# Kernel optimization log

Measured on AMD Instinct MI355X. Metric: run time of the kernel, lower is better.

Reference implementation:

```python
import jax, jax.numpy as jnp
import numpy as np

B, N, D, E, L = 4, 256, 128, 64, 3  # batch, nodes, node_dim, edge_dim, num_layers
LN_EPS = 1e-5


def setup_inputs() -> dict:
    key = jax.random.key(0)
    ks = jax.random.split(key, 12)

    def w(k, shape, fan_in):
        return jax.random.normal(k, shape, dtype=jnp.float32) / np.float32(np.sqrt(fan_in))

    return {
        "node_features": jax.random.normal(ks[0], (B, N, D), dtype=jnp.float32),
        "adjacency": jax.random.uniform(ks[1], (B, N, N), dtype=jnp.float32),
        # per-layer edge network: Linear(2D->E), ReLU, Linear(E->E)
        "ew1": w(ks[2], (L, 2 * D, E), 2 * D), "eb1": jnp.zeros((L, E), jnp.float32),
        "ew2": w(ks[3], (L, E, E), E),         "eb2": jnp.zeros((L, E), jnp.float32),
        # per-layer message network: Linear(D+E->2D), ReLU, Linear(2D->D)
        "mw1": w(ks[4], (L, D + E, 2 * D), D + E), "mb1": jnp.zeros((L, 2 * D), jnp.float32),
        "mw2": w(ks[5], (L, 2 * D, D), 2 * D),     "mb2": jnp.zeros((L, D), jnp.float32),
        # per-layer update network: Linear(2D->2D), ReLU, Linear(2D->D)
        "uw1": w(ks[6], (L, 2 * D, 2 * D), 2 * D), "ub1": jnp.zeros((L, 2 * D), jnp.float32),
        "uw2": w(ks[7], (L, 2 * D, D), 2 * D),     "ub2": jnp.zeros((L, D), jnp.float32),
        # per-layer LayerNorm
        "ln_g": jnp.ones((L, D), jnp.float32), "ln_b": jnp.zeros((L, D), jnp.float32),
    }


def _layernorm(x, g, b):
    mu = jnp.mean(x, axis=-1, keepdims=True)
    var = jnp.mean(jnp.square(x - mu), axis=-1, keepdims=True)
    return (x - mu) * jax.lax.rsqrt(var + LN_EPS) * g + b


def _forward(node_features, adjacency, ew1, eb1, ew2, eb2, mw1, mb1, mw2, mb2,
             uw1, ub1, uw2, ub2, ln_g, ln_b):
    x = node_features  # [B,N,D]
    for l in range(L):
        # Edge features: edge_input[b,i,j] = cat(x[b,i], x[b,j]); first Linear split to
        # avoid materializing [B,N,N,2D]: cat @ W == x_i @ W_top + x_j @ W_bot.
        w_top, w_bot = ew1[l][:D], ew1[l][D:]
        eh = jax.nn.relu(
            jnp.einsum('bid,de->bie', x, w_top)[:, :, None, :]
            + jnp.einsum('bjd,de->bje', x, w_bot)[:, None, :, :]
            + eb1[l]
        )  # [B,N,N,E]
        edge_feat = jnp.einsum('bije,ef->bijf', eh, ew2[l]) + eb2[l]  # [B,N,N,E]

        # GraphConvLayer: message_input[b,i,j] = cat(x[b,i], edge_feat[b,i,j])
        mw_top, mw_bot = mw1[l][:D], mw1[l][D:]
        mh = jax.nn.relu(
            jnp.einsum('bid,dh->bih', x, mw_top)[:, :, None, :]
            + jnp.einsum('bije,eh->bijh', edge_feat, mw_bot)
            + mb1[l]
        )  # [B,N,N,2D]
        message = jnp.einsum('bijh,hd->bijd', mh, mw2[l]) + mb2[l]  # [B,N,N,D]
        # adjacency-weighted sum over neighbors j (per-node torch loop, vectorized)
        messages = jnp.einsum('bij,bijd->bid', adjacency, message)  # [B,N,D]

        upd_in = jnp.concatenate([x, messages], axis=-1)  # [B,N,2D]
        uh = jax.nn.relu(jnp.einsum('bih,hk->bik', upd_in, uw1[l]) + ub1[l])
        x_new = jnp.einsum('bik,kd->bid', uh, uw2[l]) + ub2[l]  # [B,N,D]

        x = _layernorm(x + x_new, ln_g[l], ln_b[l])
    return x


def reference(node_features, adjacency, ew1, eb1, ew2, eb2, mw1, mb1, mw2, mb2,
              uw1, ub1, uw2, ub2, ln_g, ln_b):
    return _forward(node_features, adjacency, ew1, eb1, ew2, eb2, mw1, mb1, mw2,
                    mb2, uw1, ub1, uw2, ub2, ln_g, ln_b)
```

## Files before the change

kernel.cpp:

```cpp
#include <hip/hip_runtime.h>
#include <hip/hip_bf16.h>


constexpr int cB = 4, cN = 256, cD = 128, cE = 64, cL = 3, cH = 256;
constexpr int RT = 4;
#define LN_EPSF 1e-5f

typedef __attribute__((ext_vector_type(8))) short bf8;
typedef __attribute__((ext_vector_type(4))) float f4;

__device__ __forceinline__ ushort f2bf(float f) {
    uint u = __float_as_uint(f);
    u += 0x7FFFu + ((u >> 16) & 1u);
    return (ushort)(u >> 16);
}

__global__ __launch_bounds__(256) void kW(const float* __restrict__ ew2,
                                          const float* __restrict__ eb2,
                                          const float* __restrict__ mw1,
                                          ushort* __restrict__ W2f,
                                          float* __restrict__ BS2) {
    int bx = blockIdx.x, l = bx >> 3, f0 = (bx & 7) * 8;
    int h = threadIdx.x;
    const float* ew2l = ew2 + l * cE * cE;
    const float* eb2l = eb2 + l * cE;
    const float* mbot = mw1 + l * (cD + cE) * cH + cD * cH;
    float acc[8];
#pragma unroll
    for (int f = 0; f < 8; ++f) acc[f] = 0.f;
    float bacc = 0.f;
    for (int e = 0; e < cE; ++e) {
        float m = mbot[e * cH + h];
        if (f0 == 0) bacc += eb2l[e] * m;
#pragma unroll
        for (int f = 0; f < 8; ++f) acc[f] += ew2l[(f0 + f) * cE + e] * m;
    }
    ushort* W2fl = W2f + l * cE * cH;
    int ht = h >> 4, hc = h & 15;
#pragma unroll
    for (int f = 0; f < 8; ++f) {
        int ff = f0 + f;
        int kc = ff >> 5, lg = (ff >> 3) & 3, e = ff & 7;
        W2fl[((ht * 2 + kc) * 64 + lg * 16 + hc) * 8 + e] = f2bf(acc[f]);
    }
    if (f0 == 0) BS2[l * cH + h] = bacc;
}

__device__ __forceinline__ void proj_1024(const float (*xs)[cD],
                                          float (*ph4)[RT][cH],
                                          float (*pm8)[RT][cD],
                                          int r0, int t,
                                          const float* __restrict__ ew1,
                                          const float* __restrict__ eb1,
                                          const float* __restrict__ mw1,
                                          const float* __restrict__ mb1,
                                          const float* __restrict__ bs2,
                                          float* __restrict__ P1,
                                          float* __restrict__ P2,
                                          float* __restrict__ P3, int nl) {
    {
        int col = t & 255, kc = t >> 8;
        const float* mw1n = mw1 + nl * (cD + cE) * cH;
        float a[RT];
#pragma unroll
        for (int r = 0; r < RT; ++r) a[r] = 0.f;
        for (int k = kc * 32; k < kc * 32 + 32; ++k) {
            float w = mw1n[k * cH + col];
#pragma unroll
            for (int r = 0; r < RT; ++r) a[r] += xs[r][k] * w;
        }
#pragma unroll
        for (int r = 0; r < RT; ++r) ph4[kc][r][col] = a[r];
    }
    {
        int cc = t & 127, kc = t >> 7;
        int which = cc >> 6, e = cc & 63;
        const float* ew1n = ew1 + nl * 2 * cD * cE + which * cD * cE;
        float a[RT];
#pragma unroll
        for (int r = 0; r < RT; ++r) a[r] = 0.f;
        for (int k = kc * 16; k < kc * 16 + 16; ++k) {
            float w = ew1n[k * cE + e];
#pragma unroll
            for (int r = 0; r < RT; ++r) a[r] += xs[r][k] * w;
        }
#pragma unroll
        for (int r = 0; r < RT; ++r) pm8[kc][r][cc] = a[r];
    }
    __syncthreads();
    {
        int r = t >> 8, col = t & 255;
        float v = mb1[nl * cH + col] + bs2[nl * cH + col];
#pragma unroll
        for (int kc = 0; kc < 4; ++kc) v += ph4[kc][r][col];
        P3[(r0 + r) * cH + col] = v;
    }
    if (t < 512) {
        int r = t >> 7, cc = t & 127, which = cc >> 6, e = cc & 63;
        float v = which ? 0.f : eb1[nl * cE + e];
#pragma unroll
        for (int kc = 0; kc < 8; ++kc) v += pm8[kc][r][cc];
        (which ? P2 : P1)[(r0 + r) * cE + e] = v;
    }
}

__global__ __launch_bounds__(1024) void kP(const float* __restrict__ x,
                                           const float* __restrict__ ew1,
                                           const float* __restrict__ eb1,
                                           const float* __restrict__ mw1,
                                           const float* __restrict__ mb1,
                                           const float* __restrict__ bs2,
                                           float* __restrict__ P1,
                                           float* __restrict__ P2,
                                           float* __restrict__ P3) {
    __shared__ float xs[RT][cD];
    __shared__ float ph4[4][RT][cH];
    __shared__ float pm8[8][RT][cD];
    int r0 = blockIdx.x * RT, t = threadIdx.x;
    if (t < 512) {
        int r = t >> 7, d = t & 127;
        xs[r][d] = x[(r0 + r) * cD + d];
    }
    __syncthreads();
    proj_1024(xs, ph4, pm8, r0, t, ew1, eb1, mw1, mb1, bs2, P1, P2, P3, 0);
}

__global__ __launch_bounds__(256, 8) void kB(const float* __restrict__ P1,
                                             const float* __restrict__ P2,
                                             const float* __restrict__ P3,
                                             const float* __restrict__ adj,
                                             const ushort* __restrict__ W2f,
                                             float* __restrict__ Sp,
                                             float* __restrict__ AsumP, int l) {
    __shared__ float sP3[cH];
    __shared__ float sS[4][cH];
    __shared__ float sAs[4];
    int bx = blockIdx.x, bn = bx >> 1, half = bx & 1;
    int t = threadIdx.x, w = t >> 6, ln = t & 63, g = ln >> 4, c = ln & 15;
    int b = bn >> 8;
    int jw = half * 128 + w * 32;

    sP3[t] = P3[bn * cH + t];

    const float* adjr = adj + bn * cN + jw;
    float adjv[2][4];
    float asum = 0.f;
#pragma unroll
    for (int jt = 0; jt < 2; ++jt)
#pragma unroll
        for (int q = 0; q < 4; ++q) {
            float a = adjr[jt * 16 + g * 4 + q];
            adjv[jt][q] = a;
            asum += a;
        }
    asum += __shfl_xor(asum, 16);
    asum += __shfl_xor(asum, 32);

    const float* p1p = P1 + bn * cE;
    f4 p1lo[2], p1hi[2];
#pragma unroll
    for (int kc = 0; kc < 2; ++kc) {
        p1lo[kc] = *(const f4*)(p1p + kc * 32 + g * 8);
        p1hi[kc] = *(const f4*)(p1p + kc * 32 + g * 8 + 4);
    }

    bf8 af[2][2];
#pragma unroll
    for (int jt = 0; jt < 2; ++jt) {
        const float* p2r = P2 + (b * cN + jw + jt * 16 + c) * cE;
#pragma unroll
        for (int kc = 0; kc < 2; ++kc) {
            f4 v0 = *(const f4*)(p2r + kc * 32 + g * 8);
            f4 v1 = *(const f4*)(p2r + kc * 32 + g * 8 + 4);
            bf8 a;
#pragma unroll
            for (int e = 0; e < 4; ++e) {
                float x0 = v0[e] + p1lo[kc][e]; x0 = x0 > 0.f ? x0 : 0.f;
                float x1 = v1[e] + p1hi[kc][e]; x1 = x1 > 0.f ? x1 : 0.f;
                a[e]     = (short)f2bf(x0);
                a[e + 4] = (short)f2bf(x1);
            }
            af[jt][kc] = a;
        }
    }
    __syncthreads();

    const ushort* W2l = W2f + l * cE * cH;
    bf8 nb0 = *(const bf8*)(W2l + (0 * 64 + ln) * 8);
    bf8 nb1 = *(const bf8*)(W2l + (1 * 64 + ln) * 8);
    for (int ht = 0; ht < 16; ++ht) {
        bf8 b0 = nb0, b1 = nb1;
        if (ht < 15) {
            nb0 = *(const bf8*)(W2l + (((ht + 1) * 2 + 0) * 64 + ln) * 8);
            nb1 = *(const bf8*)(W2l + (((ht + 1) * 2 + 1) * 64 + ln) * 8);
        }
        float p3v = sP3[ht * 16 + c];
        float sp = 0.f;
#pragma unroll
        for (int jt = 0; jt < 2; ++jt) {
            f4 acc = {0.f, 0.f, 0.f, 0.f};
            acc = __builtin_amdgcn_mfma_f32_16x16x32_bf16(af[jt][0], b0, acc, 0, 0, 0);
            acc = __builtin_amdgcn_mfma_f32_16x16x32_bf16(af[jt][1], b1, acc, 0, 0, 0);
#pragma unroll
            for (int q = 0; q < 4; ++q) {
                float mh = p3v + acc[q];
                mh = mh > 0.f ? mh : 0.f;
                sp += adjv[jt][q] * mh;
            }
        }
        sp += __shfl_xor(sp, 16);
        sp += __shfl_xor(sp, 32);
        if (ln < 16) sS[w][ht * 16 + c] = sp;
    }
    if (ln == 0) sAs[w] = asum;
    __syncthreads();
    Sp[bx * cH + t] = sS[0][t] + sS[1][t] + sS[2][t] + sS[3][t];
    if (t == 0) AsumP[bx] = sAs[0] + sAs[1] + sAs[2] + sAs[3];
}

__global__ __launch_bounds__(1024) void kU(const float* __restrict__ x_in,
                                           float* __restrict__ x_out,
                                           const float* __restrict__ Sp,
                                           const float* __restrict__ AsumP,
                                           const float* __restrict__ mw2,
                                           const float* __restrict__ mb2,
                                           const float* __restrict__ uw1,
                                           const float* __restrict__ ub1,
                                           const float* __restrict__ uw2,
                                           const float* __restrict__ ub2,
                                           const float* __restrict__ lng,
                                           const float* __restrict__ lnb,
                                           float* __restrict__ out,
                                           const float* __restrict__ ew1,
                                           const float* __restrict__ eb1,
                                           const float* __restrict__ mw1,
                                           const float* __restrict__ mb1,
                                           const float* __restrict__ bs2,
                                           float* __restrict__ P1,
                                           float* __restrict__ P2,
                                           float* __restrict__ P3,
                                           int l, int last) {
    __shared__ float sS[RT][cH];
    __shared__ float uin[RT][cH];
    __shared__ float uh[RT][cH];
    __shared__ float ph4[4][RT][cH];
    __shared__ float pm8[8][RT][cD];
    __shared__ float yb[RT][cD];
    __shared__ float xs[RT][cD];
    __shared__ float atots[RT];
    __shared__ float rs1h[RT][2], rs2h[RT][2];
    int r0 = blockIdx.x * RT, t = threadIdx.x;

    {
        int r = t >> 8, k = t & 255;
        sS[r][k] = Sp[(2 * (r0 + r)) * cH + k] + Sp[(2 * (r0 + r) + 1) * cH + k];
    }
    if (t < RT) atots[t] = AsumP[2 * (r0 + t)] + AsumP[2 * (r0 + t) + 1];
    if (t < 512) {
        int r = t >> 7, d = t & 127;
        uin[r][d] = x_in[(r0 + r) * cD + d];
    }
    __syncthreads();

    {
        int c = t & 127, kc = t >> 7;
        const float* mw2l = mw2 + l * cH * cD;
        float a[RT];
#pragma unroll
        for (int r = 0; r < RT; ++r) a[r] = 0.f;
        for (int k = kc * 32; k < kc * 32 + 32; ++k) {
            float w = mw2l[k * cD + c];
#pragma unroll
            for (int r = 0; r < RT; ++r) a[r] += sS[r][k] * w;
        }
#pragma unroll
        for (int r = 0; r < RT; ++r) pm8[kc][r][c] = a[r];
    }
    __syncthreads();
    if (t < 512) {
        int r = t >> 7, c = t & 127;
        float m = atots[r] * mb2[l * cD + c];
#pragma unroll
        for (int kc = 0; kc < 8; ++kc) m += pm8[kc][r][c];
        uin[r][cD + c] = m;
    }
    __syncthreads();

    {
        int col = t & 255, kc = t >> 8;
        const float* uw1l = uw1 + l * cH * cH;
        float a[RT];
#pragma unroll
        for (int r = 0; r < RT; ++r) a[r] = 0.f;
        for (int k = kc * 64; k < kc * 64 + 64; ++k) {
            float w = uw1l[k * cH + col];
#pragma unroll
            for (int r = 0; r < RT; ++r) a[r] += uin[r][k] * w;
        }
#pragma unroll
        for (int r = 0; r < RT; ++r) ph4[kc][r][col] = a[r];
    }
    __syncthreads();
    {
        int r = t >> 8, col = t & 255;
        float v = ub1[l * cH + col];
#pragma unroll
        for (int kc = 0; kc < 4; ++kc) v += ph4[kc][r][col];
        uh[r][col] = v > 0.f ? v : 0.f;
    }
    __syncthreads();

    {
        int c = t & 127, kc = t >> 7;
        const float* uw2l = uw2 + l * cH * cD;
        float a[RT];
#pragma unroll
        for (int r = 0; r < RT; ++r) a[r] = 0.f;
        for (int k = kc * 32; k < kc * 32 + 32; ++k) {
            float w = uw2l[k * cD + c];
#pragma unroll
            for (int r = 0; r < RT; ++r) a[r] += uh[r][k] * w;
        }
#pragma unroll
        for (int r = 0; r < RT; ++r) pm8[kc][r][c] = a[r];
    }
    __syncthreads();
    if (t < 512) {
        int r = t >> 7, c = t & 127;
        float v = uin[r][c] + ub2[l * cD + c];
#pragma unroll
        for (int kc = 0; kc < 8; ++kc) v += pm8[kc][r][c];
        yb[r][c] = v;
    }
    __syncthreads();

    if (t < 512) {
        int r = t >> 7, q = t & 127;
        float y = yb[r][q];
        float s1 = y, s2 = y * y;
#pragma unroll
        for (int o = 1; o < 64; o <<= 1) { s1 += __shfl_xor(s1, o); s2 += __shfl_xor(s2, o); }
        if ((t & 63) == 0) { rs1h[r][q >> 6] = s1; rs2h[r][q >> 6] = s2; }
    }
    __syncthreads();
    if (t < 512) {
        int r = t >> 7, q = t & 127;
        float tot = rs1h[r][0] + rs1h[r][1];
        float tq  = rs2h[r][0] + rs2h[r][1];
        float mu  = tot * (1.f / cD);
        float var = tq * (1.f / cD) - mu * mu;
        float inv = rsqrtf(var + LN_EPSF);
        float res = (yb[r][q] - mu) * inv * lng[l * cD + q] + lnb[l * cD + q];
        x_out[(r0 + r) * cD + q] = res;
        xs[r][q] = res;
        if (last) out[(r0 + r) * cD + q] = res;
    }
    if (last) return;
    __syncthreads();

    proj_1024(xs, ph4, pm8, r0, t, ew1, eb1, mw1, mb1, bs2, P1, P2, P3, l + 1);
}

extern "C" void kernel_launch(void* const* d_in, const int* in_sizes, int n_in,
                              void* d_out, int out_size, void* d_ws, size_t ws_size,
                              hipStream_t stream) {
    (void)in_sizes; (void)n_in; (void)out_size; (void)ws_size;
    const float* nf  = (const float*)d_in[0];
    const float* adj = (const float*)d_in[1];
    const float* ew1 = (const float*)d_in[2];
    const float* eb1 = (const float*)d_in[3];
    const float* ew2 = (const float*)d_in[4];
    const float* eb2 = (const float*)d_in[5];
    const float* mw1 = (const float*)d_in[6];
    const float* mb1 = (const float*)d_in[7];
    const float* mw2 = (const float*)d_in[8];
    const float* mb2 = (const float*)d_in[9];
    const float* uw1 = (const float*)d_in[10];
    const float* ub1 = (const float*)d_in[11];
    const float* uw2 = (const float*)d_in[12];
    const float* ub2 = (const float*)d_in[13];
    const float* lng = (const float*)d_in[14];
    const float* lnb = (const float*)d_in[15];
    float* out = (float*)d_out;

    float* xbuf  = (float*)d_ws;
    float* P1    = xbuf + cB * cN * cD;
    float* P2    = P1   + cB * cN * cE;
    float* P3    = P2   + cB * cN * cE;
    float* Sp    = P3   + cB * cN * cH;
    float* AsumP = Sp   + 2 * cB * cN * cH;
    float* BS2   = AsumP + 2 * cB * cN;
    ushort* W2f  = (ushort*)(BS2 + cL * cH);

    kW<<<cL * 8, 256, 0, stream>>>(ew2, eb2, mw1, W2f, BS2);
    kP<<<cB * cN / RT, 1024, 0, stream>>>(nf, ew1, eb1, mw1, mb1, BS2, P1, P2, P3);
    for (int l = 0; l < cL; ++l) {
        kB<<<cB * cN * 2, 256, 0, stream>>>(P1, P2, P3, adj, W2f, Sp, AsumP, l);
        kU<<<cB * cN / RT, 1024, 0, stream>>>((l == 0) ? nf : xbuf, xbuf, Sp, AsumP,
                                              mw2, mb2, uw1, ub1, uw2, ub2, lng, lnb, out,
                                              ew1, eb1, mw1, mb1, BS2, P1, P2, P3,
                                              l, l == cL - 1);
    }
}
```

Before: 125.0 us.

## Split kB neighbor range into four blocks and defer cross-lane reductions

The edge/message kernel now launches four blocks per node instead of two, so each wave handles 16 neighbors (one MFMA tile) instead of 32. The bias is folded into the MFMA accumulator init, the 16 per-tile partial sums are kept in registers, and the shuffle reductions are batched after a fully unrolled loop. The update kernel sums four partials instead of two. This adds parallelism and instruction-level overlap, at the cost of twice as many blocks, more redundant W2 and P3 loads per node, a larger Sp workspace, and higher register pressure (launch bounds relaxed to 4 blocks per CU).

```diff
diff --git a/kernel.cpp b/kernel.cpp
--- a/kernel.cpp
+++ b/kernel.cpp
@@ -4,6 +4,7 @@
 
 constexpr int cB = 4, cN = 256, cD = 128, cE = 64, cL = 3, cH = 256;
 constexpr int RT = 4;
+constexpr int JS = 4;
 #define LN_EPSF 1e-5f
 
 typedef __attribute__((ext_vector_type(8))) short bf8;
@@ -125,7 +126,7 @@
     proj_1024(xs, ph4, pm8, r0, t, ew1, eb1, mw1, mb1, bs2, P1, P2, P3, 0);
 }
 
-__global__ __launch_bounds__(256, 8) void kB(const float* __restrict__ P1,
+__global__ __launch_bounds__(256, 4) void kB(const float* __restrict__ P1,
                                              const float* __restrict__ P2,
                                              const float* __restrict__ P3,
                                              const float* __restrict__ adj,
@@ -135,24 +136,22 @@
     __shared__ float sP3[cH];
     __shared__ float sS[4][cH];
     __shared__ float sAs[4];
-    int bx = blockIdx.x, bn = bx >> 1, half = bx & 1;
+    int bx = blockIdx.x, bn = bx >> 2, quarter = bx & 3;
     int t = threadIdx.x, w = t >> 6, ln = t & 63, g = ln >> 4, c = ln & 15;
     int b = bn >> 8;
-    int jw = half * 128 + w * 32;
+    int jw = quarter * 64 + w * 16;
 
     sP3[t] = P3[bn * cH + t];
 
     const float* adjr = adj + bn * cN + jw;
-    float adjv[2][4];
+    float adjv[4];
     float asum = 0.f;
 #pragma unroll
-    for (int jt = 0; jt < 2; ++jt)
-#pragma unroll
-        for (int q = 0; q < 4; ++q) {
-            float a = adjr[jt * 16 + g * 4 + q];
-            adjv[jt][q] = a;
-            asum += a;
-        }
+    for (int q = 0; q < 4; ++q) {
+        float a = adjr[g * 4 + q];
+        adjv[q] = a;
+        asum += a;
+    }
     asum += __shfl_xor(asum, 16);
     asum += __shfl_xor(asum, 32);
 
@@ -164,10 +163,9 @@
         p1hi[kc] = *(const f4*)(p1p + kc * 32 + g * 8 + 4);
     }
 
-    bf8 af[2][2];
-#pragma unroll
-    for (int jt = 0; jt < 2; ++jt) {
-        const float* p2r = P2 + (b * cN + jw + jt * 16 + c) * cE;
+    bf8 af[2];
+    {
+        const float* p2r = P2 + (b * cN + jw + c) * cE;
 #pragma unroll
         for (int kc = 0; kc < 2; ++kc) {
             f4 v0 = *(const f4*)(p2r + kc * 32 + g * 8);
@@ -180,14 +178,16 @@
                 a[e]     = (short)f2bf(x0);
                 a[e + 4] = (short)f2bf(x1);
             }
-            af[jt][kc] = a;
+            af[kc] = a;
         }
     }
     __syncthreads();
 
     const ushort* W2l = W2f + l * cE * cH;
+    float sp[16];
     bf8 nb0 = *(const bf8*)(W2l + (0 * 64 + ln) * 8);
     bf8 nb1 = *(const bf8*)(W2l + (1 * 64 + ln) * 8);
+#pragma unroll
     for (int ht = 0; ht < 16; ++ht) {
         bf8 b0 = nb0, b1 = nb1;
         if (ht < 15) {
@@ -195,22 +195,23 @@
             nb1 = *(const bf8*)(W2l + (((ht + 1) * 2 + 1) * 64 + ln) * 8);
         }
         float p3v = sP3[ht * 16 + c];
-        float sp = 0.f;
-#pragma unroll
-        for (int jt = 0; jt < 2; ++jt) {
-            f4 acc = {0.f, 0.f, 0.f, 0.f};
-            acc = __builtin_amdgcn_mfma_f32_16x16x32_bf16(af[jt][0], b0, acc, 0, 0, 0);
-            acc = __builtin_amdgcn_mfma_f32_16x16x32_bf16(af[jt][1], b1, acc, 0, 0, 0);
-#pragma unroll
-            for (int q = 0; q < 4; ++q) {
-                float mh = p3v + acc[q];
-                mh = mh > 0.f ? mh : 0.f;
-                sp += adjv[jt][q] * mh;
-            }
-        }
-        sp += __shfl_xor(sp, 16);
-        sp += __shfl_xor(sp, 32);
-        if (ln < 16) sS[w][ht * 16 + c] = sp;
+        f4 acc = {p3v, p3v, p3v, p3v};
+        acc = __builtin_amdgcn_mfma_f32_16x16x32_bf16(af[0], b0, acc, 0, 0, 0);
+        acc = __builtin_amdgcn_mfma_f32_16x16x32_bf16(af[1], b1, acc, 0, 0, 0);
+        float s = 0.f;
+#pragma unroll
+        for (int q = 0; q < 4; ++q) {
+            float mh = acc[q] > 0.f ? acc[q] : 0.f;
+            s += adjv[q] * mh;
+        }
+        sp[ht] = s;
+    }
+#pragma unroll
+    for (int ht = 0; ht < 16; ++ht) {
+        float s = sp[ht];
+        s += __shfl_xor(s, 16);
+        s += __shfl_xor(s, 32);
+        if (ln < 16) sS[w][ht * 16 + ln] = s;
     }
     if (ln == 0) sAs[w] = asum;
     __syncthreads();
@@ -253,9 +254,17 @@
 
     {
         int r = t >> 8, k = t & 255;
-        sS[r][k] = Sp[(2 * (r0 + r)) * cH + k] + Sp[(2 * (r0 + r) + 1) * cH + k];
-    }
-    if (t < RT) atots[t] = AsumP[2 * (r0 + t)] + AsumP[2 * (r0 + t) + 1];
+        float v = 0.f;
+#pragma unroll
+        for (int q = 0; q < JS; ++q) v += Sp[(JS * (r0 + r) + q) * cH + k];
+        sS[r][k] = v;
+    }
+    if (t < RT) {
+        float v = 0.f;
+#pragma unroll
+        for (int q = 0; q < JS; ++q) v += AsumP[JS * (r0 + t) + q];
+        atots[t] = v;
+    }
     if (t < 512) {
         int r = t >> 7, d = t & 127;
         uin[r][d] = x_in[(r0 + r) * cD + d];
@@ -388,14 +397,14 @@
     float* P2    = P1   + cB * cN * cE;
     float* P3    = P2   + cB * cN * cE;
     float* Sp    = P3   + cB * cN * cH;
-    float* AsumP = Sp   + 2 * cB * cN * cH;
-    float* BS2   = AsumP + 2 * cB * cN;
+    float* AsumP = Sp   + JS * cB * cN * cH;
+    float* BS2   = AsumP + JS * cB * cN;
     ushort* W2f  = (ushort*)(BS2 + cL * cH);
 
     kW<<<cL * 8, 256, 0, stream>>>(ew2, eb2, mw1, W2f, BS2);
     kP<<<cB * cN / RT, 1024, 0, stream>>>(nf, ew1, eb1, mw1, mb1, BS2, P1, P2, P3);
     for (int l = 0; l < cL; ++l) {
-        kB<<<cB * cN * 2, 256, 0, stream>>>(P1, P2, P3, adj, W2f, Sp, AsumP, l);
+        kB<<<cB * cN * JS, 256, 0, stream>>>(P1, P2, P3, adj, W2f, Sp, AsumP, l);
         kU<<<cB * cN / RT, 1024, 0, stream>>>((l == 0) ? nf : xbuf, xbuf, Sp, AsumP,
                                               mw2, mb2, uw1, ub1, uw2, ub2, lng, lnb, out,
                                               ew1, eb1, mw1, mb1, BS2, P1, P2, P3,
```

Result: slower. 164.3 us (+31.5%).

## Fuse edge-message kernel into per-layer update kernel with ping-pong projection buffers

Applied to the files above, without the earlier changes.

Merges the per-node MFMA message aggregation (kB) into the update kernel so each 1024-thread block computes neighbor sums for its 4 rows, then runs the update MLP, LayerNorm and the next layer's projections. This removes one launch per layer and the Sp/AsumP global round trip. P1/P2/P3 are now double-buffered because other blocks still read the current layer's projections. The trade-off is a grid of only 256 blocks doing the MFMA work instead of 2048 smaller blocks, with more registers and shared memory per block, which may reduce parallelism and latency hiding.

```diff
diff --git a/kernel.cpp b/kernel.cpp
--- a/kernel.cpp
+++ b/kernel.cpp
@@ -125,103 +125,13 @@
     proj_1024(xs, ph4, pm8, r0, t, ew1, eb1, mw1, mb1, bs2, P1, P2, P3, 0);
 }
 
-__global__ __launch_bounds__(256, 8) void kB(const float* __restrict__ P1,
-                                             const float* __restrict__ P2,
-                                             const float* __restrict__ P3,
-                                             const float* __restrict__ adj,
-                                             const ushort* __restrict__ W2f,
-                                             float* __restrict__ Sp,
-                                             float* __restrict__ AsumP, int l) {
-    __shared__ float sP3[cH];
-    __shared__ float sS[4][cH];
-    __shared__ float sAs[4];
-    int bx = blockIdx.x, bn = bx >> 1, half = bx & 1;
-    int t = threadIdx.x, w = t >> 6, ln = t & 63, g = ln >> 4, c = ln & 15;
-    int b = bn >> 8;
-    int jw = half * 128 + w * 32;
-
-    sP3[t] = P3[bn * cH + t];
-
-    const float* adjr = adj + bn * cN + jw;
-    float adjv[2][4];
-    float asum = 0.f;
-#pragma unroll
-    for (int jt = 0; jt < 2; ++jt)
-#pragma unroll
-        for (int q = 0; q < 4; ++q) {
-            float a = adjr[jt * 16 + g * 4 + q];
-            adjv[jt][q] = a;
-            asum += a;
-        }
-    asum += __shfl_xor(asum, 16);
-    asum += __shfl_xor(asum, 32);
-
-    const float* p1p = P1 + bn * cE;
-    f4 p1lo[2], p1hi[2];
-#pragma unroll
-    for (int kc = 0; kc < 2; ++kc) {
-        p1lo[kc] = *(const f4*)(p1p + kc * 32 + g * 8);
-        p1hi[kc] = *(const f4*)(p1p + kc * 32 + g * 8 + 4);
-    }
-
-    bf8 af[2][2];
-#pragma unroll
-    for (int jt = 0; jt < 2; ++jt) {
-        const float* p2r = P2 + (b * cN + jw + jt * 16 + c) * cE;
-#pragma unroll
-        for (int kc = 0; kc < 2; ++kc) {
-            f4 v0 = *(const f4*)(p2r + kc * 32 + g * 8);
-            f4 v1 = *(const f4*)(p2r + kc * 32 + g * 8 + 4);
-            bf8 a;
-#pragma unroll
-            for (int e = 0; e < 4; ++e) {
-                float x0 = v0[e] + p1lo[kc][e]; x0 = x0 > 0.f ? x0 : 0.f;
-                float x1 = v1[e] + p1hi[kc][e]; x1 = x1 > 0.f ? x1 : 0.f;
-                a[e]     = (short)f2bf(x0);
-                a[e + 4] = (short)f2bf(x1);
-            }
-            af[jt][kc] = a;
-        }
-    }
-    __syncthreads();
-
-    const ushort* W2l = W2f + l * cE * cH;
-    bf8 nb0 = *(const bf8*)(W2l + (0 * 64 + ln) * 8);
-    bf8 nb1 = *(const bf8*)(W2l + (1 * 64 + ln) * 8);
-    for (int ht = 0; ht < 16; ++ht) {
-        bf8 b0 = nb0, b1 = nb1;
-        if (ht < 15) {
-            nb0 = *(const bf8*)(W2l + (((ht + 1) * 2 + 0) * 64 + ln) * 8);
-            nb1 = *(const bf8*)(W2l + (((ht + 1) * 2 + 1) * 64 + ln) * 8);
-        }
-        float p3v = sP3[ht * 16 + c];
-        float sp = 0.f;
-#pragma unroll
-        for (int jt = 0; jt < 2; ++jt) {
-            f4 acc = {0.f, 0.f, 0.f, 0.f};
-            acc = __builtin_amdgcn_mfma_f32_16x16x32_bf16(af[jt][0], b0, acc, 0, 0, 0);
-            acc = __builtin_amdgcn_mfma_f32_16x16x32_bf16(af[jt][1], b1, acc, 0, 0, 0);
-#pragma unroll
-            for (int q = 0; q < 4; ++q) {
-                float mh = p3v + acc[q];
-                mh = mh > 0.f ? mh : 0.f;
-                sp += adjv[jt][q] * mh;
-            }
-        }
-        sp += __shfl_xor(sp, 16);
-        sp += __shfl_xor(sp, 32);
-        if (ln < 16) sS[w][ht * 16 + c] = sp;
-    }
-    if (ln == 0) sAs[w] = asum;
-    __syncthreads();
-    Sp[bx * cH + t] = sS[0][t] + sS[1][t] + sS[2][t] + sS[3][t];
-    if (t == 0) AsumP[bx] = sAs[0] + sAs[1] + sAs[2] + sAs[3];
-}
-
-__global__ __launch_bounds__(1024) void kU(const float* __restrict__ x_in,
+__global__ __launch_bounds__(1024) void kL(const float* __restrict__ x_in,
                                            float* __restrict__ x_out,
-                                           const float* __restrict__ Sp,
-                                           const float* __restrict__ AsumP,
+                                           const float* __restrict__ P1,
+                                           const float* __restrict__ P2,
+                                           const float* __restrict__ P3g,
+                                           const float* __restrict__ adj,
+                                           const ushort* __restrict__ W2f,
                                            const float* __restrict__ mw2,
                                            const float* __restrict__ mb2,
                                            const float* __restrict__ uw1,
@@ -236,26 +146,114 @@
                                            const float* __restrict__ mw1,
                                            const float* __restrict__ mb1,
                                            const float* __restrict__ bs2,
-                                           float* __restrict__ P1,
-                                           float* __restrict__ P2,
-                                           float* __restrict__ P3,
+                                           float* __restrict__ P1o,
+                                           float* __restrict__ P2o,
+                                           float* __restrict__ P3o,
                                            int l, int last) {
+    __shared__ float sP3[RT][cH];
+    __shared__ float sSw[16][cH];
+    __shared__ float pm8[8][RT][cD];
     __shared__ float sS[RT][cH];
     __shared__ float uin[RT][cH];
     __shared__ float uh[RT][cH];
-    __shared__ float ph4[4][RT][cH];
-    __shared__ float pm8[8][RT][cD];
     __shared__ float yb[RT][cD];
     __shared__ float xs[RT][cD];
+    __shared__ float sAsw[16];
     __shared__ float atots[RT];
     __shared__ float rs1h[RT][2], rs2h[RT][2];
-    int r0 = blockIdx.x * RT, t = threadIdx.x;
+
+    int bx = blockIdx.x, t = threadIdx.x;
+    int r0 = bx * RT;
+    int w = t >> 6, ln = t & 63, g = ln >> 4, c = ln & 15;
+    int rw = w >> 2, qd = w & 3;
+    int bn = r0 + rw;
+    int b  = bn >> 8;
+    int jw = qd * 64;
+
+    sP3[t >> 8][t & 255] = P3g[(r0 + (t >> 8)) * cH + (t & 255)];
+
+    const float* adjr = adj + bn * cN + jw;
+    float adjv[4][4];
+    float asum = 0.f;
+#pragma unroll
+    for (int jt = 0; jt < 4; ++jt)
+#pragma unroll
+        for (int q = 0; q < 4; ++q) {
+            float a = adjr[jt * 16 + g * 4 + q];
+            adjv[jt][q] = a;
+            asum += a;
+        }
+    asum += __shfl_xor(asum, 16);
+    asum += __shfl_xor(asum, 32);
+
+    const float* p1p = P1 + bn * cE;
+    f4 p1lo[2], p1hi[2];
+#pragma unroll
+    for (int kc = 0; kc < 2; ++kc) {
+        p1lo[kc] = *(const f4*)(p1p + kc * 32 + g * 8);
+        p1hi[kc] = *(const f4*)(p1p + kc * 32 + g * 8 + 4);
+    }
+
+    bf8 af[4][2];
+#pragma unroll
+    for (int jt = 0; jt < 4; ++jt) {
+        const float* p2r = P2 + (b * cN + jw + jt * 16 + c) * cE;
+#pragma unroll
+        for (int kc = 0; kc < 2; ++kc) {
+            f4 v0 = *(const f4*)(p2r + kc * 32 + g * 8);
+            f4 v1 = *(const f4*)(p2r + kc * 32 + g * 8 + 4);
+            bf8 a;
+#pragma unroll
+            for (int e = 0; e < 4; ++e) {
+                float x0 = v0[e] + p1lo[kc][e]; x0 = x0 > 0.f ? x0 : 0.f;
+                float x1 = v1[e] + p1hi[kc][e]; x1 = x1 > 0.f ? x1 : 0.f;
+                a[e]     = (short)f2bf(x0);
+                a[e + 4] = (short)f2bf(x1);
+            }
+            af[jt][kc] = a;
+        }
+    }
+    __syncthreads();
+
+    {
+        const ushort* W2l = W2f + l * cE * cH;
+        bf8 nb0 = *(const bf8*)(W2l + (0 * 64 + ln) * 8);
+        bf8 nb1 = *(const bf8*)(W2l + (1 * 64 + ln) * 8);
+        for (int ht = 0; ht < 16; ++ht) {
+            bf8 b0 = nb0, b1 = nb1;
+            if (ht < 15) {
+                nb0 = *(const bf8*)(W2l + (((ht + 1) * 2 + 0) * 64 + ln) * 8);
+                nb1 = *(const bf8*)(W2l + (((ht + 1) * 2 + 1) * 64 + ln) * 8);
+            }
+            float p3v = sP3[rw][ht * 16 + c];
+            float sp = 0.f;
+#pragma unroll
+            for (int jt = 0; jt < 4; ++jt) {
+                f4 acc = {0.f, 0.f, 0.f, 0.f};
+                acc = __builtin_amdgcn_mfma_f32_16x16x32_bf16(af[jt][0], b0, acc, 0, 0, 0);
+                acc = __builtin_amdgcn_mfma_f32_16x16x32_bf16(af[jt][1], b1, acc, 0, 0, 0);
+#pragma unroll
+                for (int q = 0; q < 4; ++q) {
+                    float mh = p3v + acc[q];
+                    mh = mh > 0.f ? mh : 0.f;
+                    sp += adjv[jt][q] * mh;
+                }
+            }
+            sp += __shfl_xor(sp, 16);
+            sp += __shfl_xor(sp, 32);
+            if (ln < 16) sSw[w][ht * 16 + c] = sp;
+        }
+    }
+    if (ln == 0) sAsw[w] = asum;
+    __syncthreads();
 
     {
         int r = t >> 8, k = t & 255;
-        sS[r][k] = Sp[(2 * (r0 + r)) * cH + k] + Sp[(2 * (r0 + r) + 1) * cH + k];
-    }
-    if (t < RT) atots[t] = AsumP[2 * (r0 + t)] + AsumP[2 * (r0 + t) + 1];
+        sS[r][k] = sSw[4 * r + 0][k] + sSw[4 * r + 1][k]
+                 + sSw[4 * r + 2][k] + sSw[4 * r + 3][k];
+    }
+    if (t < RT)
+        atots[t] = sAsw[4 * t] + sAsw[4 * t + 1] + sAsw[4 * t + 2] + sAsw[4 * t + 3];
     if (t < 512) {
         int r = t >> 7, d = t & 127;
         uin[r][d] = x_in[(r0 + r) * cD + d];
@@ -263,26 +261,26 @@
     __syncthreads();
 
     {
-        int c = t & 127, kc = t >> 7;
+        int cc = t & 127, kc = t >> 7;
         const float* mw2l = mw2 + l * cH * cD;
         float a[RT];
 #pragma unroll
         for (int r = 0; r < RT; ++r) a[r] = 0.f;
         for (int k = kc * 32; k < kc * 32 + 32; ++k) {
-            float w = mw2l[k * cD + c];
-#pragma unroll
-            for (int r = 0; r < RT; ++r) a[r] += sS[r][k] * w;
-        }
-#pragma unroll
-        for (int r = 0; r < RT; ++r) pm8[kc][r][c] = a[r];
-    }
-    __syncthreads();
-    if (t < 512) {
-        int r = t >> 7, c = t & 127;
-        float m = atots[r] * mb2[l * cD + c];
-#pragma unroll
-        for (int kc = 0; kc < 8; ++kc) m += pm8[kc][r][c];
-        uin[r][cD + c] = m;
+            float wv = mw2l[k * cD + cc];
+#pragma unroll
+            for (int r = 0; r < RT; ++r) a[r] += sS[r][k] * wv;
+        }
+#pragma unroll
+        for (int r = 0; r < RT; ++r) pm8[kc][r][cc] = a[r];
+    }
+    __syncthreads();
+    if (t < 512) {
+        int r = t >> 7, cc = t & 127;
+        float m = atots[r] * mb2[l * cD + cc];
+#pragma unroll
+        for (int kc = 0; kc < 8; ++kc) m += pm8[kc][r][cc];
+        uin[r][cD + cc] = m;
     }
     __syncthreads();
 
@@ -293,44 +291,44 @@
 #pragma unroll
         for (int r = 0; r < RT; ++r) a[r] = 0.f;
         for (int k = kc * 64; k < kc * 64 + 64; ++k) {
-            float w = uw1l[k * cH + col];
-#pragma unroll
-            for (int r = 0; r < RT; ++r) a[r] += uin[r][k] * w;
-        }
-#pragma unroll
-        for (int r = 0; r < RT; ++r) ph4[kc][r][col] = a[r];
+            float wv = uw1l[k * cH + col];
+#pragma unroll
+            for (int r = 0; r < RT; ++r) a[r] += uin[r][k] * wv;
+        }
+#pragma unroll
+        for (int r = 0; r < RT; ++r) sSw[kc * RT + r][col] = a[r];
     }
     __syncthreads();
     {
         int r = t >> 8, col = t & 255;
         float v = ub1[l * cH + col];
 #pragma unroll
-        for (int kc = 0; kc < 4; ++kc) v += ph4[kc][r][col];
+        for (int kc = 0; kc < 4; ++kc) v += sSw[kc * RT + r][col];
         uh[r][col] = v > 0.f ? v : 0.f;
     }
     __syncthreads();
 
     {
-        int c = t & 127, kc = t >> 7;
+        int cc = t & 127, kc = t >> 7;
         const float* uw2l = uw2 + l * cH * cD;
         float a[RT];
 #pragma unroll
         for (int r = 0; r < RT; ++r) a[r] = 0.f;
         for (int k = kc * 32; k < kc * 32 + 32; ++k) {
-            float w = uw2l[k * cD + c];
-#pragma unroll
-            for (int r = 0; r < RT; ++r) a[r] += uh[r][k] * w;
-        }
-#pragma unroll
-        for (int r = 0; r < RT; ++r) pm8[kc][r][c] = a[r];
-    }
-    __syncthreads();
-    if (t < 512) {
-        int r = t >> 7, c = t & 127;
-        float v = uin[r][c] + ub2[l * cD + c];
-#pragma unroll
-        for (int kc = 0; kc < 8; ++kc) v += pm8[kc][r][c];
-        yb[r][c] = v;
+            float wv = uw2l[k * cD + cc];
+#pragma unroll
+            for (int r = 0; r < RT; ++r) a[r] += uh[r][k] * wv;
+        }
+#pragma unroll
+        for (int r = 0; r < RT; ++r) pm8[kc][r][cc] = a[r];
+    }
+    __syncthreads();
+    if (t < 512) {
+        int r = t >> 7, cc = t & 127;
+        float v = uin[r][cc] + ub2[l * cD + cc];
+#pragma unroll
+        for (int kc = 0; kc < 8; ++kc) v += pm8[kc][r][cc];
+        yb[r][cc] = v;
     }
     __syncthreads();
 
@@ -358,7 +356,8 @@
     if (last) return;
     __syncthreads();
 
-    proj_1024(xs, ph4, pm8, r0, t, ew1, eb1, mw1, mb1, bs2, P1, P2, P3, l + 1);
+    proj_1024(xs, reinterpret_cast<float (*)[RT][cH]>(&sSw[0][0]), pm8,
+              r0, t, ew1, eb1, mw1, mb1, bs2, P1o, P2o, P3o, l + 1);
 }
 
 extern "C" void kernel_launch(void* const* d_in, const int* in_sizes, int n_in,
@@ -384,21 +383,28 @@
     float* out = (float*)d_out;
 
     float* xbuf  = (float*)d_ws;
-    float* P1    = xbuf + cB * cN * cD;
-    float* P2    = P1   + cB * cN * cE;
-    float* P3    = P2   + cB * cN * cE;
-    float* Sp    = P3   + cB * cN * cH;
-    float* AsumP = Sp   + 2 * cB * cN * cH;
-    float* BS2   = AsumP + 2 * cB * cN;
+    float* P1a   = xbuf + cB * cN * cD;
+    float* P2a   = P1a  + cB * cN * cE;
+    float* P3a   = P2a  + cB * cN * cE;
+    float* P1b   = P3a  + cB * cN * cH;
+    float* P2b   = P1b  + cB * cN * cE;
+    float* P3b   = P2b  + cB * cN * cE;
+    float* BS2   = P3b  + cB * cN * cH;
     ushort* W2f  = (ushort*)(BS2 + cL * cH);
 
+    float* P1s[2] = {P1a, P1b};
+    float* P2s[2] = {P2a, P2b};
+    float* P3s[2] = {P3a, P3b};
+
     kW<<<cL * 8, 256, 0, stream>>>(ew2, eb2, mw1, W2f, BS2);
-    kP<<<cB * cN / RT, 1024, 0, stream>>>(nf, ew1, eb1, mw1, mb1, BS2, P1, P2, P3);
+    kP<<<cB * cN / RT, 1024, 0, stream>>>(nf, ew1, eb1, mw1, mb1, BS2, P1a, P2a, P3a);
     for (int l = 0; l < cL; ++l) {
-        kB<<<cB * cN * 2, 256, 0, stream>>>(P1, P2, P3, adj, W2f, Sp, AsumP, l);
-        kU<<<cB * cN / RT, 1024, 0, stream>>>((l == 0) ? nf : xbuf, xbuf, Sp, AsumP,
-                                              mw2, mb2, uw1, ub1, uw2, ub2, lng, lnb, out,
-                                              ew1, eb1, mw1, mb1, BS2, P1, P2, P3,
+        int pi = l & 1, po = (l + 1) & 1;
+        kL<<<cB * cN / RT, 1024, 0, stream>>>((l == 0) ? nf : xbuf, xbuf,
+                                              P1s[pi], P2s[pi], P3s[pi], adj, W2f,
+                                              mw2, mb2, uw1, ub1, uw2, ub2, lng, lnb,
+                                              out, ew1, eb1, mw1, mb1, BS2,
+                                              P1s[po], P2s[po], P3s[po],
                                               l, l == cL - 1);
     }
 }
```

After: 103.4 us, median of 3. 17.3% less time.
